# Kernel tuning notes

Hardware: AMD Instinct MI355X
Metric: run time of the kernel (lower is better)

The kernel has to match this reference:

```python
import jax, jax.numpy as jnp
import numpy as np

N_NODES = 100000
N_EDGES = 3200000
N_FEAT = 512
HIDDEN = 16
N_LABELS = 64


def gcn_layer(x, frm, to, W, b, n_nodes):
    # Original removes existing self-loops then adds one self-loop per node.
    # Equivalent jit-friendly form: zero-mask self-loop edges, add +1 to every
    # node's degree and an explicit self-loop term deg^-0.5 * deg^-0.5 * xw.
    mask = (frm != to).astype(x.dtype)                      # [E]
    deg = jax.ops.segment_sum(mask, to, num_segments=n_nodes) + 1.0  # [N], >=1 so no inf
    dis = deg ** -0.5                                        # [N]
    ew = dis[frm] * mask * dis[to]                           # [E]
    xw = x @ W                                               # [N, out]
    msgs = xw[frm] * ew[:, None]                             # gather-multiply  [E, out]
    agg = jax.ops.segment_sum(msgs, to, num_segments=n_nodes)  # scatter-add [N, out]
    out = agg + xw * (dis * dis)[:, None] + b                # self-loop weight = dis[i]^2
    return out


def setup_inputs() -> dict:
    key = jax.random.key(0)
    k1, k2, k3, k4 = jax.random.split(key, 4)
    x = jax.random.normal(k1, (N_NODES, N_FEAT), dtype=jnp.float32)
    edge_index = jax.random.randint(k2, (2, N_EDGES), 0, N_NODES, dtype=jnp.int32)
    # Xavier-uniform linear weights, zero bias (reset_paramters)
    lim1 = float(np.sqrt(6.0 / (N_FEAT + HIDDEN)))
    W1 = jax.random.uniform(k3, (N_FEAT, HIDDEN), jnp.float32, -lim1, lim1)
    b1 = jnp.zeros((HIDDEN,), jnp.float32)
    lim2 = float(np.sqrt(6.0 / (HIDDEN + N_LABELS)))
    W2 = jax.random.uniform(k4, (HIDDEN, N_LABELS), jnp.float32, -lim2, lim2)
    b2 = jnp.zeros((N_LABELS,), jnp.float32)
    return {"x": x, "edge_index": edge_index, "W1": W1, "b1": b1, "W2": W2, "b2": b2}


def reference(x, edge_index, W1, b1, W2, b2):
    n = x.shape[0]
    frm, to = edge_index[0], edge_index[1]
    h = jax.nn.relu(gcn_layer(x, frm, to, W1, b1, n))
    # dropout is identity in eval mode
    logits = gcn_layer(h, frm, to, W2, b2, n)
    return jax.nn.log_softmax(logits, axis=1)
```

## Files before the change

### kernel.cpp

```cpp
#include <hip/hip_runtime.h>
#include <hip/hip_fp16.h>
#include <cstdint>
#include <cstddef>

#define N_NODES 100000
#define N_FEAT  512
#define HIDDEN  16
#define N_LABELS 64
#define N_EDGES 3200000

#define NB    782
#define NPAD  (NB * 128)
#define CAP   4608
#define EPB   4096
#define BIN_BLOCKS 782
#define SPLITK 4
#define GBLK  196

static const size_t O_GCUR = 0;
static const size_t O_DIS  = (size_t)16 << 10;
static const size_t O_STA  = (size_t)420 << 10;
static const size_t O_END  = (size_t)824 << 10;
static const size_t O_XWS  = (size_t)1228 << 10;
static const size_t O_HS   = (size_t)4360 << 10;
static const size_t O_TMP  = (size_t)7492 << 10;
static const size_t O_PART = (size_t)21572 << 10;
#define PART_STRIDE_H ((size_t)NPAD * 16)

struct BinSh {
    unsigned short barr[EPB];
    unsigned       pk[EPB];
    int hist[NB + 1];
    int gbase[NB];
    int lcur[NB];
};
union SMemBG {
    BinSh bin;
    float xs[512 * 17];
};

__global__ __launch_bounds__(512) void k_bg(const int* __restrict__ frm,
                                            const int* __restrict__ to,
                                            int* __restrict__ gcur,
                                            unsigned* __restrict__ tmp,
                                            const float* __restrict__ x,
                                            const float* __restrict__ W1,
                                            __half* __restrict__ part) {
    __shared__ SMemBG sm;
    const int t = threadIdx.x;
    const int bid = blockIdx.x;

    if (bid < BIN_BLOCKS) {
        BinSh& B = sm.bin;
        const size_t e0 = (size_t)bid * EPB;

        for (int i = t; i < NB + 1; i += 512) B.hist[i] = 0;
        __syncthreads();

        #pragma unroll
        for (int i = t; i < EPB; i += 512) {
            size_t e = e0 + i;
            int b = NB;
            unsigned pk = 0;
            if (e < N_EDGES) {
                int f = frm[e], tt = to[e];
                if (f != tt) {
                    b = tt >> 7;
                    pk = ((unsigned)f << 7) | (unsigned)(tt & 127);
                }
            }
            B.barr[i] = (unsigned short)b;
            B.pk[i] = pk;
            atomicAdd(&B.hist[b], 1);
        }
        __syncthreads();

        for (int b = t; b < NB; b += 512) {
            B.gbase[b] = atomicAdd(&gcur[b], B.hist[b]);
            B.lcur[b] = 0;
        }
        __syncthreads();

        #pragma unroll
        for (int i = t; i < EPB; i += 512) {
            int b = B.barr[i];
            if (b < NB) {
                int r = atomicAdd(&B.lcur[b], 1);
                int p = B.gbase[b] + r;
                if (p < CAP)
                    tmp[(size_t)b * CAP + p] = B.pk[i];
            }
        }
    } else {
        const int g = bid - BIN_BLOCKS;
        const int split = g / GBLK;
        const int bx = g - split * GBLK;
        const int base = bx * 512;
        const int kb = split * 128;

        float acc[HIDDEN];
        #pragma unroll
        for (int j = 0; j < HIDDEN; ++j) acc[j] = 0.f;

        const int pr = t >> 2;
        const int pc = (t & 3) << 2;

        for (int kt = 0; kt < 8; ++kt) {
            __syncthreads();
            #pragma unroll
            for (int p = 0; p < 4; ++p) {
                int r = p * 128 + pr;
                int n = base + r;
                float4 v = make_float4(0.f, 0.f, 0.f, 0.f);
                if (n < N_NODES)
                    v = *(const float4*)(x + (size_t)n * N_FEAT + kb + kt * 16 + pc);
                sm.xs[r * 17 + pc + 0] = v.x;
                sm.xs[r * 17 + pc + 1] = v.y;
                sm.xs[r * 17 + pc + 2] = v.z;
                sm.xs[r * 17 + pc + 3] = v.w;
            }
            __syncthreads();
            #pragma unroll
            for (int kk = 0; kk < 16; ++kk) {
                float xv = sm.xs[t * 17 + kk];
                const float4* wr = (const float4*)(W1 + ((size_t)(kb + kt * 16 + kk) << 4));
                float4 wa = wr[0], wb = wr[1], wc = wr[2], wd = wr[3];
                acc[ 0] = fmaf(xv, wa.x, acc[ 0]);
                acc[ 1] = fmaf(xv, wa.y, acc[ 1]);
                acc[ 2] = fmaf(xv, wa.z, acc[ 2]);
                acc[ 3] = fmaf(xv, wa.w, acc[ 3]);
                acc[ 4] = fmaf(xv, wb.x, acc[ 4]);
                acc[ 5] = fmaf(xv, wb.y, acc[ 5]);
                acc[ 6] = fmaf(xv, wb.z, acc[ 6]);
                acc[ 7] = fmaf(xv, wb.w, acc[ 7]);
                acc[ 8] = fmaf(xv, wc.x, acc[ 8]);
                acc[ 9] = fmaf(xv, wc.y, acc[ 9]);
                acc[10] = fmaf(xv, wc.z, acc[10]);
                acc[11] = fmaf(xv, wc.w, acc[11]);
                acc[12] = fmaf(xv, wd.x, acc[12]);
                acc[13] = fmaf(xv, wd.y, acc[13]);
                acc[14] = fmaf(xv, wd.z, acc[14]);
                acc[15] = fmaf(xv, wd.w, acc[15]);
            }
        }
        int n = base + t;
        if (n < N_NODES) {
            __half2 h2[8];
            #pragma unroll
            for (int j = 0; j < 8; ++j)
                h2[j] = __float22half2_rn(make_float2(acc[2 * j], acc[2 * j + 1]));
            float4* o = (float4*)(part + (size_t)split * PART_STRIDE_H + (size_t)n * HIDDEN);
            o[0] = *(float4*)&h2[0];
            o[1] = *(float4*)&h2[4];
        }
    }
}

__global__ __launch_bounds__(512) void k_sort(unsigned* __restrict__ tmp,
                                              const int* __restrict__ gcur,
                                              int* __restrict__ starts,
                                              int* __restrict__ ends,
                                              float* __restrict__ dis) {
    __shared__ unsigned stage[CAP];
    __shared__ int cnt[128];
    __shared__ int sc[128];
    __shared__ int lcur[128];
    const int t = threadIdx.x, b = blockIdx.x;
    const int n_e = min(gcur[b], CAP);
    unsigned* seg = tmp + (size_t)b * CAP;

    if (t < 128) { cnt[t] = 0; lcur[t] = 0; }
    __syncthreads();

    for (int i = t; i < n_e; i += 512) {
        unsigned w = seg[i];
        stage[i] = w;
        atomicAdd(&cnt[w & 127u], 1);
    }
    __syncthreads();

    if (t < 128) sc[t] = cnt[t];
    __syncthreads();
    #pragma unroll
    for (int off = 1; off < 128; off <<= 1) {
        int a = 0;
        if (t < 128 && t >= off) a = sc[t - off];
        __syncthreads();
        if (t < 128) sc[t] += a;
        __syncthreads();
    }

    if (t < 128) {
        int excl = sc[t] - cnt[t];
        int node = b * 128 + t;
        int s0 = b * CAP + excl;
        starts[node] = s0;
        ends[node]   = s0 + cnt[t];
        dis[node]    = rsqrtf((float)cnt[t] + 1.0f);
    }
    __syncthreads();

    for (int i = t; i < n_e; i += 512) {
        unsigned w = stage[i];
        int tl = (int)(w & 127u);
        int p = atomicAdd(&lcur[tl], 1);
        seg[(sc[tl] - cnt[tl]) + p] = w >> 7;
    }
}

__global__ __launch_bounds__(256) void k_comb(const __half2* __restrict__ part2,
                                              const float* __restrict__ dis,
                                              __half2* __restrict__ xws2) {
    int i = blockIdx.x * 256 + threadIdx.x;
    if (i >= N_NODES * 8) return;
    const size_t st = (size_t)NPAD * 8;
    float2 a = __half22float2(part2[i]);
    float2 b = __half22float2(part2[st + i]);
    float2 c = __half22float2(part2[2 * st + i]);
    float2 d = __half22float2(part2[3 * st + i]);
    float dn = dis[i >> 3];
    xws2[i] = __float22half2_rn(make_float2(dn * (a.x + b.x + c.x + d.x),
                                            dn * (a.y + b.y + c.y + d.y)));
}

__global__ __launch_bounds__(512) void k_agg(const __half* __restrict__ rows,
                                             const unsigned* __restrict__ sorted,
                                             const int* __restrict__ starts,
                                             const int* __restrict__ ends,
                                             const float* __restrict__ dis,
                                             const float* __restrict__ bias,
                                             __half* __restrict__ outp,
                                             int mode) {
    const int t = threadIdx.x;
    const int lane = t & 15, g = t >> 4;
    const int n = blockIdx.x * 32 + g;
    const int s0 = starts[n], e0 = ends[n];
    float acc = 0.f;
    for (int base = s0; base < e0; base += 16) {
        int idx = base + lane;
        unsigned f = (idx < e0) ? sorted[idx] : 0u;
        int cnt = min(16, e0 - base);
        #pragma unroll
        for (int q = 0; q < 16; ++q) {
            unsigned fq = __shfl(f, q, 16);
            float v = __half2float(rows[(size_t)fq * HIDDEN + lane]);
            if (q < cnt) acc += v;
        }
    }
    if (n < N_NODES) {
        float dn = dis[n];
        float sum = acc + __half2float(rows[(size_t)n * HIDDEN + lane]);
        float v;
        if (mode) v = fmaxf(fmaf(dn, sum, bias[lane]), 0.f) * dn;
        else      v = dn * sum;
        outp[(size_t)n * HIDDEN + lane] = __float2half(v);
    }
}

__global__ __launch_bounds__(256) void k_out(const __half* __restrict__ z,
                                             const float* __restrict__ W2,
                                             const float* __restrict__ b2,
                                             float* __restrict__ out) {
    int gt = blockIdx.x * 256 + threadIdx.x;
    int n = gt >> 6;
    int j = gt & 63;
    float acc = b2[j];
    const __half* zr = z + (size_t)n * HIDDEN;
    #pragma unroll
    for (int k = 0; k < HIDDEN; ++k)
        acc = fmaf(__half2float(zr[k]), W2[k * N_LABELS + j], acc);
    float m = acc;
    #pragma unroll
    for (int off = 32; off > 0; off >>= 1)
        m = fmaxf(m, __shfl_xor(m, off, 64));
    float ex = __expf(acc - m);
    float sum = ex;
    #pragma unroll
    for (int off = 32; off > 0; off >>= 1)
        sum += __shfl_xor(sum, off, 64);
    out[(size_t)n * N_LABELS + j] = acc - m - __logf(sum);
}

extern "C" void kernel_launch(void* const* d_in, const int* in_sizes, int n_in,
                              void* d_out, int out_size, void* d_ws, size_t ws_size,
                              hipStream_t stream) {
    const float* x  = (const float*)d_in[0];
    const int*   ei = (const int*)d_in[1];
    const float* W1 = (const float*)d_in[2];
    const float* b1 = (const float*)d_in[3];
    const float* W2 = (const float*)d_in[4];
    const float* b2 = (const float*)d_in[5];
    float* out = (float*)d_out;
    char*  ws  = (char*)d_ws;

    int*      gcur   = (int*)(ws + O_GCUR);
    float*    dis    = (float*)(ws + O_DIS);
    int*      starts = (int*)(ws + O_STA);
    int*      ends   = (int*)(ws + O_END);
    __half*   xws    = (__half*)(ws + O_XWS);
    __half*   hs     = (__half*)(ws + O_HS);
    unsigned* tmp    = (unsigned*)(ws + O_TMP);
    __half*   part   = (__half*)(ws + O_PART);

    const int* frm = ei;
    const int* to  = ei + N_EDGES;

    hipMemsetAsync(gcur, 0, NB * sizeof(int), stream);

    k_bg   <<<BIN_BLOCKS + SPLITK * GBLK, 512, 0, stream>>>(frm, to, gcur, tmp, x, W1, part);
    k_sort <<<NB, 512, 0, stream>>>(tmp, gcur, starts, ends, dis);
    k_comb <<<3125, 256, 0, stream>>>((const __half2*)part, dis, (__half2*)xws);
    k_agg  <<<NPAD / 32, 512, 0, stream>>>(xws, tmp, starts, ends, dis, b1, hs, 1);
    k_agg  <<<NPAD / 32, 512, 0, stream>>>(hs, tmp, starts, ends, dis, b1, xws, 0);
    k_out  <<<N_NODES / 4, 256, 0, stream>>>(xws, W2, b2, out);
}
```

Measured before the change: 457.4 us.

## Replace binned sort with degree-count, block-scan offsets and global atomic scatter CSR build

Swaps the two-pass bin-then-sort CSR construction for a simpler scheme. It counts per-node in-degree with global atomics, computes per-node offsets with a block scan plus a global atomic base, then scatters source indices with per-node atomic cursors. The partial-sum combine kernel is merged into the scatter kernel as extra blocks, which saves one launch and drops the fixed CAP limit per bin. The cost is a second full read of the edge list and far more global atomics, which are contended and randomly addressed. The edge order within each node also becomes nondeterministic, and blocks receive their base offsets in arbitrary order.

Result: slower. 798.6 us (+74.6%).

```diff
diff --git a/kernel.cpp b/kernel.cpp
--- a/kernel.cpp
+++ b/kernel.cpp
@@ -11,88 +11,46 @@
 
 #define NB    782
 #define NPAD  (NB * 128)
-#define CAP   4608
 #define EPB   4096
-#define BIN_BLOCKS 782
+#define DEG_BLOCKS 782
+#define SC_BLOCKS  782
 #define SPLITK 4
 #define GBLK  196
 
-static const size_t O_GCUR = 0;
-static const size_t O_DIS  = (size_t)16 << 10;
-static const size_t O_STA  = (size_t)420 << 10;
-static const size_t O_END  = (size_t)824 << 10;
-static const size_t O_XWS  = (size_t)1228 << 10;
-static const size_t O_HS   = (size_t)4360 << 10;
-static const size_t O_TMP  = (size_t)7492 << 10;
-static const size_t O_PART = (size_t)21572 << 10;
+static const size_t O_CNT  = 0;
+static const size_t O_DEG  = (size_t)16 << 10;
+static const size_t O_DIS  = (size_t)420 << 10;
+static const size_t O_STA  = (size_t)824 << 10;
+static const size_t O_END  = (size_t)1228 << 10;
+static const size_t O_CUR  = (size_t)1632 << 10;
+static const size_t O_XWS  = (size_t)2036 << 10;
+static const size_t O_HS   = (size_t)5168 << 10;
+static const size_t O_TMP  = (size_t)8300 << 10;
+static const size_t O_PART = (size_t)20900 << 10;
 #define PART_STRIDE_H ((size_t)NPAD * 16)
-
-struct BinSh {
-    unsigned short barr[EPB];
-    unsigned       pk[EPB];
-    int hist[NB + 1];
-    int gbase[NB];
-    int lcur[NB];
-};
-union SMemBG {
-    BinSh bin;
-    float xs[512 * 17];
-};
 
 __global__ __launch_bounds__(512) void k_bg(const int* __restrict__ frm,
                                             const int* __restrict__ to,
-                                            int* __restrict__ gcur,
-                                            unsigned* __restrict__ tmp,
+                                            int* __restrict__ deg,
                                             const float* __restrict__ x,
                                             const float* __restrict__ W1,
                                             __half* __restrict__ part) {
-    __shared__ SMemBG sm;
+    __shared__ float xs[512 * 17];
     const int t = threadIdx.x;
     const int bid = blockIdx.x;
 
-    if (bid < BIN_BLOCKS) {
-        BinSh& B = sm.bin;
+    if (bid < DEG_BLOCKS) {
         const size_t e0 = (size_t)bid * EPB;
-
-        for (int i = t; i < NB + 1; i += 512) B.hist[i] = 0;
-        __syncthreads();
-
         #pragma unroll
         for (int i = t; i < EPB; i += 512) {
             size_t e = e0 + i;
-            int b = NB;
-            unsigned pk = 0;
             if (e < N_EDGES) {
                 int f = frm[e], tt = to[e];
-                if (f != tt) {
-                    b = tt >> 7;
-                    pk = ((unsigned)f << 7) | (unsigned)(tt & 127);
-                }
-            }
-            B.barr[i] = (unsigned short)b;
-            B.pk[i] = pk;
-            atomicAdd(&B.hist[b], 1);
-        }
-        __syncthreads();
-
-        for (int b = t; b < NB; b += 512) {
-            B.gbase[b] = atomicAdd(&gcur[b], B.hist[b]);
-            B.lcur[b] = 0;
-        }
-        __syncthreads();
-
-        #pragma unroll
-        for (int i = t; i < EPB; i += 512) {
-            int b = B.barr[i];
-            if (b < NB) {
-                int r = atomicAdd(&B.lcur[b], 1);
-                int p = B.gbase[b] + r;
-                if (p < CAP)
-                    tmp[(size_t)b * CAP + p] = B.pk[i];
+                if (f != tt) atomicAdd(&deg[tt], 1);
             }
         }
     } else {
-        const int g = bid - BIN_BLOCKS;
+        const int g = bid - DEG_BLOCKS;
         const int split = g / GBLK;
         const int bx = g - split * GBLK;
         const int base = bx * 512;
@@ -114,15 +72,15 @@
                 float4 v = make_float4(0.f, 0.f, 0.f, 0.f);
                 if (n < N_NODES)
                     v = *(const float4*)(x + (size_t)n * N_FEAT + kb + kt * 16 + pc);
-                sm.xs[r * 17 + pc + 0] = v.x;
-                sm.xs[r * 17 + pc + 1] = v.y;
-                sm.xs[r * 17 + pc + 2] = v.z;
-                sm.xs[r * 17 + pc + 3] = v.w;
+                xs[r * 17 + pc + 0] = v.x;
+                xs[r * 17 + pc + 1] = v.y;
+                xs[r * 17 + pc + 2] = v.z;
+                xs[r * 17 + pc + 3] = v.w;
             }
             __syncthreads();
             #pragma unroll
             for (int kk = 0; kk < 16; ++kk) {
-                float xv = sm.xs[t * 17 + kk];
+                float xv = xs[t * 17 + kk];
                 const float4* wr = (const float4*)(W1 + ((size_t)(kb + kt * 16 + kk) << 4));
                 float4 wa = wr[0], wb = wr[1], wc = wr[2], wd = wr[3];
                 acc[ 0] = fmaf(xv, wa.x, acc[ 0]);
@@ -156,75 +114,78 @@
     }
 }
 
-__global__ __launch_bounds__(512) void k_sort(unsigned* __restrict__ tmp,
-                                              const int* __restrict__ gcur,
+__global__ __launch_bounds__(128) void k_base(const int* __restrict__ deg,
+                                              int* __restrict__ cnt,
                                               int* __restrict__ starts,
                                               int* __restrict__ ends,
+                                              int* __restrict__ cur,
                                               float* __restrict__ dis) {
-    __shared__ unsigned stage[CAP];
-    __shared__ int cnt[128];
     __shared__ int sc[128];
-    __shared__ int lcur[128];
-    const int t = threadIdx.x, b = blockIdx.x;
-    const int n_e = min(gcur[b], CAP);
-    unsigned* seg = tmp + (size_t)b * CAP;
-
-    if (t < 128) { cnt[t] = 0; lcur[t] = 0; }
+    __shared__ int base;
+    const int t = threadIdx.x;
+    const int n = blockIdx.x * 128 + t;
+    const int d = deg[n];
+    sc[t] = d;
     __syncthreads();
-
-    for (int i = t; i < n_e; i += 512) {
-        unsigned w = seg[i];
-        stage[i] = w;
-        atomicAdd(&cnt[w & 127u], 1);
-    }
+    #pragma unroll
+    for (int off = 1; off < 128; off <<= 1) {
+        int a = (t >= off) ? sc[t - off] : 0;
+        __syncthreads();
+        sc[t] += a;
+        __syncthreads();
+    }
+    if (t == 127) base = atomicAdd(cnt, sc[127]);
     __syncthreads();
-
-    if (t < 128) sc[t] = cnt[t];
-    __syncthreads();
-    #pragma unroll
-    for (int off = 1; off < 128; off <<= 1) {
-        int a = 0;
-        if (t < 128 && t >= off) a = sc[t - off];
-        __syncthreads();
-        if (t < 128) sc[t] += a;
-        __syncthreads();
-    }
-
-    if (t < 128) {
-        int excl = sc[t] - cnt[t];
-        int node = b * 128 + t;
-        int s0 = b * CAP + excl;
-        starts[node] = s0;
-        ends[node]   = s0 + cnt[t];
-        dis[node]    = rsqrtf((float)cnt[t] + 1.0f);
-    }
-    __syncthreads();
-
-    for (int i = t; i < n_e; i += 512) {
-        unsigned w = stage[i];
-        int tl = (int)(w & 127u);
-        int p = atomicAdd(&lcur[tl], 1);
-        seg[(sc[tl] - cnt[tl]) + p] = w >> 7;
-    }
-}
-
-__global__ __launch_bounds__(256) void k_comb(const __half2* __restrict__ part2,
-                                              const float* __restrict__ dis,
-                                              __half2* __restrict__ xws2) {
-    int i = blockIdx.x * 256 + threadIdx.x;
-    if (i >= N_NODES * 8) return;
-    const size_t st = (size_t)NPAD * 8;
-    float2 a = __half22float2(part2[i]);
-    float2 b = __half22float2(part2[st + i]);
-    float2 c = __half22float2(part2[2 * st + i]);
-    float2 d = __half22float2(part2[3 * st + i]);
-    float dn = dis[i >> 3];
-    xws2[i] = __float22half2_rn(make_float2(dn * (a.x + b.x + c.x + d.x),
-                                            dn * (a.y + b.y + c.y + d.y)));
+    const int s0 = base + sc[t] - d;
+    starts[n] = s0;
+    ends[n]   = s0 + d;
+    cur[n]    = s0;
+    dis[n]    = rsqrtf((float)d + 1.0f);
+}
+
+__global__ __launch_bounds__(512) void k_sc(const int* __restrict__ frm,
+                                            const int* __restrict__ to,
+                                            int* __restrict__ cur,
+                                            int* __restrict__ tmp,
+                                            const __half2* __restrict__ part2,
+                                            const float* __restrict__ dis,
+                                            __half2* __restrict__ xws2) {
+    const int t = threadIdx.x;
+    const int bid = blockIdx.x;
+    if (bid < SC_BLOCKS) {
+        const size_t e0 = (size_t)bid * EPB;
+        #pragma unroll
+        for (int i = t; i < EPB; i += 512) {
+            size_t e = e0 + i;
+            if (e < N_EDGES) {
+                int f = frm[e], tt = to[e];
+                if (f != tt) {
+                    int p = atomicAdd(&cur[tt], 1);
+                    tmp[p] = f;
+                }
+            }
+        }
+    } else {
+        const int g = bid - SC_BLOCKS;
+        const size_t st = (size_t)NPAD * 8;
+        int i = g * 512 + t;
+        #pragma unroll
+        for (int rep = 0; rep < 2; ++rep, i += SC_BLOCKS * 512) {
+            if (i < N_NODES * 8) {
+                float2 a = __half22float2(part2[i]);
+                float2 b = __half22float2(part2[st + i]);
+                float2 c = __half22float2(part2[2 * st + i]);
+                float2 d = __half22float2(part2[3 * st + i]);
+                float dn = dis[i >> 3];
+                xws2[i] = __float22half2_rn(make_float2(dn * (a.x + b.x + c.x + d.x),
+                                                        dn * (a.y + b.y + c.y + d.y)));
+            }
+        }
+    }
 }
 
 __global__ __launch_bounds__(512) void k_agg(const __half* __restrict__ rows,
-                                             const unsigned* __restrict__ sorted,
+                                             const int* __restrict__ sorted,
                                              const int* __restrict__ starts,
                                              const int* __restrict__ ends,
                                              const float* __restrict__ dis,
@@ -238,7 +199,7 @@
     float acc = 0.f;
     for (int base = s0; base < e0; base += 16) {
         int idx = base + lane;
-        unsigned f = (idx < e0) ? sorted[idx] : 0u;
+        unsigned f = (idx < e0) ? (unsigned)sorted[idx] : 0u;
         int cnt = min(16, e0 - base);
         #pragma unroll
         for (int q = 0; q < 16; ++q) {
@@ -293,23 +254,26 @@
     float* out = (float*)d_out;
     char*  ws  = (char*)d_ws;
 
-    int*      gcur   = (int*)(ws + O_GCUR);
+    int*      cnt    = (int*)(ws + O_CNT);
+    int*      deg    = (int*)(ws + O_DEG);
     float*    dis    = (float*)(ws + O_DIS);
     int*      starts = (int*)(ws + O_STA);
     int*      ends   = (int*)(ws + O_END);
+    int*      cur    = (int*)(ws + O_CUR);
     __half*   xws    = (__half*)(ws + O_XWS);
     __half*   hs     = (__half*)(ws + O_HS);
-    unsigned* tmp    = (unsigned*)(ws + O_TMP);
+    int*      tmp    = (int*)(ws + O_TMP);
     __half*   part   = (__half*)(ws + O_PART);
 
     const int* frm = ei;
     const int* to  = ei + N_EDGES;
 
-    hipMemsetAsync(gcur, 0, NB * sizeof(int), stream);
-
-    k_bg   <<<BIN_BLOCKS + SPLITK * GBLK, 512, 0, stream>>>(frm, to, gcur, tmp, x, W1, part);
-    k_sort <<<NB, 512, 0, stream>>>(tmp, gcur, starts, ends, dis);
-    k_comb <<<3125, 256, 0, stream>>>((const __half2*)part, dis, (__half2*)xws);
+    hipMemsetAsync(ws, 0, O_DEG + (size_t)NPAD * sizeof(int), stream);
+
+    k_bg   <<<DEG_BLOCKS + SPLITK * GBLK, 512, 0, stream>>>(frm, to, deg, x, W1, part);
+    k_base <<<NB, 128, 0, stream>>>(deg, cnt, starts, ends, cur, dis);
+    k_sc   <<<SC_BLOCKS * 2, 512, 0, stream>>>(frm, to, cur, tmp,
+                                               (const __half2*)part, dis, (__half2*)xws);
     k_agg  <<<NPAD / 32, 512, 0, stream>>>(xws, tmp, starts, ends, dis, b1, hs, 1);
     k_agg  <<<NPAD / 32, 512, 0, stream>>>(hs, tmp, starts, ends, dis, b1, xws, 0);
     k_out  <<<N_NODES / 4, 256, 0, stream>>>(xws, W2, b2, out);
```

## Drop per-node sort; aggregate bucketed edges via shared-memory atomics

Applied to the files above, without the earlier changes.

Removes the k_sort kernel that counting-sorted each 128-node bucket into CSR order. k_agg now works one block per bucket: it walks the unsorted edges and accumulates gathered rows into a padded shared-memory tile with atomics. Node degrees are now counted with global atomics during binning, and the normalisation factor is recomputed from them where needed. This saves a kernel launch and a global read/write pass over the edges. In exchange it adds 3.2M global atomics in k_bg and shared-memory atomic contention in both aggregation passes, and k_agg launches far fewer, larger blocks (782 instead of about 3100).

After: 1.134 ms. 148% more time.

```diff
diff --git a/kernel.cpp b/kernel.cpp
--- a/kernel.cpp
+++ b/kernel.cpp
@@ -18,13 +18,11 @@
 #define GBLK  196
 
 static const size_t O_GCUR = 0;
-static const size_t O_DIS  = (size_t)16 << 10;
-static const size_t O_STA  = (size_t)420 << 10;
-static const size_t O_END  = (size_t)824 << 10;
-static const size_t O_XWS  = (size_t)1228 << 10;
-static const size_t O_HS   = (size_t)4360 << 10;
-static const size_t O_TMP  = (size_t)7492 << 10;
-static const size_t O_PART = (size_t)21572 << 10;
+static const size_t O_DEG  = (size_t)16 << 10;
+static const size_t O_XWS  = (size_t)420 << 10;
+static const size_t O_HS   = (size_t)3560 << 10;
+static const size_t O_TMP  = (size_t)6700 << 10;
+static const size_t O_PART = (size_t)20800 << 10;
 #define PART_STRIDE_H ((size_t)NPAD * 16)
 
 struct BinSh {
@@ -42,6 +40,7 @@
 __global__ __launch_bounds__(512) void k_bg(const int* __restrict__ frm,
                                             const int* __restrict__ to,
                                             int* __restrict__ gcur,
+                                            int* __restrict__ deg,
                                             unsigned* __restrict__ tmp,
                                             const float* __restrict__ x,
                                             const float* __restrict__ W1,
@@ -67,6 +66,7 @@
                 if (f != tt) {
                     b = tt >> 7;
                     pk = ((unsigned)f << 7) | (unsigned)(tt & 127);
+                    atomicAdd(&deg[tt], 1);
                 }
             }
             B.barr[i] = (unsigned short)b;
@@ -156,60 +156,8 @@
     }
 }
 
-__global__ __launch_bounds__(512) void k_sort(unsigned* __restrict__ tmp,
-                                              const int* __restrict__ gcur,
-                                              int* __restrict__ starts,
-                                              int* __restrict__ ends,
-                                              float* __restrict__ dis) {
-    __shared__ unsigned stage[CAP];
-    __shared__ int cnt[128];
-    __shared__ int sc[128];
-    __shared__ int lcur[128];
-    const int t = threadIdx.x, b = blockIdx.x;
-    const int n_e = min(gcur[b], CAP);
-    unsigned* seg = tmp + (size_t)b * CAP;
-
-    if (t < 128) { cnt[t] = 0; lcur[t] = 0; }
-    __syncthreads();
-
-    for (int i = t; i < n_e; i += 512) {
-        unsigned w = seg[i];
-        stage[i] = w;
-        atomicAdd(&cnt[w & 127u], 1);
-    }
-    __syncthreads();
-
-    if (t < 128) sc[t] = cnt[t];
-    __syncthreads();
-    #pragma unroll
-    for (int off = 1; off < 128; off <<= 1) {
-        int a = 0;
-        if (t < 128 && t >= off) a = sc[t - off];
-        __syncthreads();
-        if (t < 128) sc[t] += a;
-        __syncthreads();
-    }
-
-    if (t < 128) {
-        int excl = sc[t] - cnt[t];
-        int node = b * 128 + t;
-        int s0 = b * CAP + excl;
-        starts[node] = s0;
-        ends[node]   = s0 + cnt[t];
-        dis[node]    = rsqrtf((float)cnt[t] + 1.0f);
-    }
-    __syncthreads();
-
-    for (int i = t; i < n_e; i += 512) {
-        unsigned w = stage[i];
-        int tl = (int)(w & 127u);
-        int p = atomicAdd(&lcur[tl], 1);
-        seg[(sc[tl] - cnt[tl]) + p] = w >> 7;
-    }
-}
-
 __global__ __launch_bounds__(256) void k_comb(const __half2* __restrict__ part2,
-                                              const float* __restrict__ dis,
+                                              const int* __restrict__ deg,
                                               __half2* __restrict__ xws2) {
     int i = blockIdx.x * 256 + threadIdx.x;
     if (i >= N_NODES * 8) return;
@@ -218,42 +166,48 @@
     float2 b = __half22float2(part2[st + i]);
     float2 c = __half22float2(part2[2 * st + i]);
     float2 d = __half22float2(part2[3 * st + i]);
-    float dn = dis[i >> 3];
+    float dn = rsqrtf((float)deg[i >> 3] + 1.0f);
     xws2[i] = __float22half2_rn(make_float2(dn * (a.x + b.x + c.x + d.x),
                                             dn * (a.y + b.y + c.y + d.y)));
 }
 
 __global__ __launch_bounds__(512) void k_agg(const __half* __restrict__ rows,
-                                             const unsigned* __restrict__ sorted,
-                                             const int* __restrict__ starts,
-                                             const int* __restrict__ ends,
-                                             const float* __restrict__ dis,
+                                             const unsigned* __restrict__ tmp,
+                                             const int* __restrict__ gcur,
+                                             const int* __restrict__ deg,
                                              const float* __restrict__ bias,
                                              __half* __restrict__ outp,
                                              int mode) {
+    __shared__ float acc[128 * 17];
     const int t = threadIdx.x;
+    const int b = blockIdx.x;
+    const int n_e = min(gcur[b], CAP);
+    const unsigned* seg = tmp + (size_t)b * CAP;
+
+    #pragma unroll
+    for (int i = t; i < 128 * 17; i += 512) acc[i] = 0.f;
+    __syncthreads();
+
     const int lane = t & 15, g = t >> 4;
-    const int n = blockIdx.x * 32 + g;
-    const int s0 = starts[n], e0 = ends[n];
-    float acc = 0.f;
-    for (int base = s0; base < e0; base += 16) {
-        int idx = base + lane;
-        unsigned f = (idx < e0) ? sorted[idx] : 0u;
-        int cnt = min(16, e0 - base);
-        #pragma unroll
-        for (int q = 0; q < 16; ++q) {
-            unsigned fq = __shfl(f, q, 16);
-            float v = __half2float(rows[(size_t)fq * HIDDEN + lane]);
-            if (q < cnt) acc += v;
-        }
+    for (int i = g; i < n_e; i += 32) {
+        unsigned w = seg[i];
+        float v = __half2float(rows[(size_t)(w >> 7) * HIDDEN + lane]);
+        atomicAdd(&acc[(w & 127u) * 17 + lane], v);
     }
-    if (n < N_NODES) {
-        float dn = dis[n];
-        float sum = acc + __half2float(rows[(size_t)n * HIDDEN + lane]);
-        float v;
-        if (mode) v = fmaxf(fmaf(dn, sum, bias[lane]), 0.f) * dn;
-        else      v = dn * sum;
-        outp[(size_t)n * HIDDEN + lane] = __float2half(v);
+    __syncthreads();
+
+    #pragma unroll
+    for (int i = t; i < 2048; i += 512) {
+        int nl = i >> 4, ln = i & 15;
+        int n = b * 128 + nl;
+        if (n < N_NODES) {
+            float dn = rsqrtf((float)deg[n] + 1.0f);
+            float sum = acc[nl * 17 + ln] + __half2float(rows[(size_t)n * HIDDEN + ln]);
+            float v;
+            if (mode) v = fmaxf(fmaf(dn, sum, bias[ln]), 0.f) * dn;
+            else      v = dn * sum;
+            outp[(size_t)n * HIDDEN + ln] = __float2half(v);
+        }
     }
 }
 
@@ -293,24 +247,21 @@
     float* out = (float*)d_out;
     char*  ws  = (char*)d_ws;
 
-    int*      gcur   = (int*)(ws + O_GCUR);
-    float*    dis    = (float*)(ws + O_DIS);
-    int*      starts = (int*)(ws + O_STA);
-    int*      ends   = (int*)(ws + O_END);
-    __half*   xws    = (__half*)(ws + O_XWS);
-    __half*   hs     = (__half*)(ws + O_HS);
-    unsigned* tmp    = (unsigned*)(ws + O_TMP);
-    __half*   part   = (__half*)(ws + O_PART);
+    int*      gcur = (int*)(ws + O_GCUR);
+    int*      deg  = (int*)(ws + O_DEG);
+    __half*   xws  = (__half*)(ws + O_XWS);
+    __half*   hs   = (__half*)(ws + O_HS);
+    unsigned* tmp  = (unsigned*)(ws + O_TMP);
+    __half*   part = (__half*)(ws + O_PART);
 
     const int* frm = ei;
     const int* to  = ei + N_EDGES;
 
-    hipMemsetAsync(gcur, 0, NB * sizeof(int), stream);
-
-    k_bg   <<<BIN_BLOCKS + SPLITK * GBLK, 512, 0, stream>>>(frm, to, gcur, tmp, x, W1, part);
-    k_sort <<<NB, 512, 0, stream>>>(tmp, gcur, starts, ends, dis);
-    k_comb <<<3125, 256, 0, stream>>>((const __half2*)part, dis, (__half2*)xws);
-    k_agg  <<<NPAD / 32, 512, 0, stream>>>(xws, tmp, starts, ends, dis, b1, hs, 1);
-    k_agg  <<<NPAD / 32, 512, 0, stream>>>(hs, tmp, starts, ends, dis, b1, xws, 0);
+    hipMemsetAsync(ws, 0, O_DEG + (size_t)NPAD * sizeof(int), stream);
+
+    k_bg   <<<BIN_BLOCKS + SPLITK * GBLK, 512, 0, stream>>>(frm, to, gcur, deg, tmp, x, W1, part);
+    k_comb <<<3125, 256, 0, stream>>>((const __half2*)part, deg, (__half2*)xws);
+    k_agg  <<<NB, 512, 0, stream>>>(xws, tmp, gcur, deg, b1, hs, 1);
+    k_agg  <<<NB, 512, 0, stream>>>(hs, tmp, gcur, deg, b1, xws, 0);
     k_out  <<<N_NODES / 4, 256, 0, stream>>>(xws, W2, b2, out);
 }
```

## Fuse second aggregation with output linear and log-softmax; reuse histogram rank

Applied to the files above, without the earlier changes.

The second aggregation kernel now also does the 16x64 output projection, bias and log-softmax in registers using sub-warp shuffles. This removes the separate output kernel and the round trip of the intermediate half-precision node features through global memory. The binning phase also records each edge's rank from the histogram atomic, so the second shared-memory atomic pass and the lcur array go away. The cost is an extra rank array in shared memory, and the fused kernel does more work per thread.

Result: faster. 445.6 us (-2.6%).

```diff
diff --git a/kernel.cpp b/kernel.cpp
--- a/kernel.cpp
+++ b/kernel.cpp
@@ -29,10 +29,10 @@
 
 struct BinSh {
     unsigned short barr[EPB];
+    unsigned short rank[EPB];
     unsigned       pk[EPB];
     int hist[NB + 1];
     int gbase[NB];
-    int lcur[NB];
 };
 union SMemBG {
     BinSh bin;
@@ -69,24 +69,22 @@
                     pk = ((unsigned)f << 7) | (unsigned)(tt & 127);
                 }
             }
+            int r = atomicAdd(&B.hist[b], 1);
             B.barr[i] = (unsigned short)b;
-            B.pk[i] = pk;
-            atomicAdd(&B.hist[b], 1);
-        }
-        __syncthreads();
-
-        for (int b = t; b < NB; b += 512) {
+            B.rank[i] = (unsigned short)r;
+            B.pk[i]   = pk;
+        }
+        __syncthreads();
+
+        for (int b = t; b < NB; b += 512)
             B.gbase[b] = atomicAdd(&gcur[b], B.hist[b]);
-            B.lcur[b] = 0;
-        }
         __syncthreads();
 
         #pragma unroll
         for (int i = t; i < EPB; i += 512) {
             int b = B.barr[i];
             if (b < NB) {
-                int r = atomicAdd(&B.lcur[b], 1);
-                int p = B.gbase[b] + r;
+                int p = B.gbase[b] + (int)B.rank[i];
                 if (p < CAP)
                     tmp[(size_t)b * CAP + p] = B.pk[i];
             }
@@ -223,14 +221,13 @@
                                             dn * (a.y + b.y + c.y + d.y)));
 }
 
-__global__ __launch_bounds__(512) void k_agg(const __half* __restrict__ rows,
-                                             const unsigned* __restrict__ sorted,
-                                             const int* __restrict__ starts,
-                                             const int* __restrict__ ends,
-                                             const float* __restrict__ dis,
-                                             const float* __restrict__ bias,
-                                             __half* __restrict__ outp,
-                                             int mode) {
+__global__ __launch_bounds__(512) void k_agg1(const __half* __restrict__ rows,
+                                              const unsigned* __restrict__ sorted,
+                                              const int* __restrict__ starts,
+                                              const int* __restrict__ ends,
+                                              const float* __restrict__ dis,
+                                              const float* __restrict__ bias,
+                                              __half* __restrict__ outp) {
     const int t = threadIdx.x;
     const int lane = t & 15, g = t >> 4;
     const int n = blockIdx.x * 32 + g;
@@ -250,35 +247,65 @@
     if (n < N_NODES) {
         float dn = dis[n];
         float sum = acc + __half2float(rows[(size_t)n * HIDDEN + lane]);
-        float v;
-        if (mode) v = fmaxf(fmaf(dn, sum, bias[lane]), 0.f) * dn;
-        else      v = dn * sum;
+        float v = fmaxf(fmaf(dn, sum, bias[lane]), 0.f) * dn;
         outp[(size_t)n * HIDDEN + lane] = __float2half(v);
     }
 }
 
-__global__ __launch_bounds__(256) void k_out(const __half* __restrict__ z,
-                                             const float* __restrict__ W2,
-                                             const float* __restrict__ b2,
-                                             float* __restrict__ out) {
-    int gt = blockIdx.x * 256 + threadIdx.x;
-    int n = gt >> 6;
-    int j = gt & 63;
-    float acc = b2[j];
-    const __half* zr = z + (size_t)n * HIDDEN;
+__global__ __launch_bounds__(512) void k_agg2o(const __half* __restrict__ rows,
+                                               const unsigned* __restrict__ sorted,
+                                               const int* __restrict__ starts,
+                                               const int* __restrict__ ends,
+                                               const float* __restrict__ dis,
+                                               const float* __restrict__ W2,
+                                               const float* __restrict__ b2,
+                                               float* __restrict__ out) {
+    const int t = threadIdx.x;
+    const int lane = t & 15, g = t >> 4;
+    const int n = blockIdx.x * 32 + g;
+    const int s0 = starts[n], e0 = ends[n];
+    float acc = 0.f;
+    for (int base = s0; base < e0; base += 16) {
+        int idx = base + lane;
+        unsigned f = (idx < e0) ? sorted[idx] : 0u;
+        int cnt = min(16, e0 - base);
+        #pragma unroll
+        for (int q = 0; q < 16; ++q) {
+            unsigned fq = __shfl(f, q, 16);
+            float v = __half2float(rows[(size_t)fq * HIDDEN + lane]);
+            if (q < cnt) acc += v;
+        }
+    }
+    float dn = (n < N_NODES) ? dis[n] : 1.f;
+    float z = dn * (acc + __half2float(rows[(size_t)n * HIDDEN + lane]));
+
+    float o0 = b2[lane], o1 = b2[lane + 16], o2 = b2[lane + 32], o3 = b2[lane + 48];
     #pragma unroll
-    for (int k = 0; k < HIDDEN; ++k)
-        acc = fmaf(__half2float(zr[k]), W2[k * N_LABELS + j], acc);
-    float m = acc;
+    for (int k = 0; k < HIDDEN; ++k) {
+        float zk = __shfl(z, k, 16);
+        const float* wr = W2 + k * N_LABELS;
+        o0 = fmaf(zk, wr[lane],      o0);
+        o1 = fmaf(zk, wr[lane + 16], o1);
+        o2 = fmaf(zk, wr[lane + 32], o2);
+        o3 = fmaf(zk, wr[lane + 48], o3);
+    }
+    float m = fmaxf(fmaxf(o0, o1), fmaxf(o2, o3));
     #pragma unroll
-    for (int off = 32; off > 0; off >>= 1)
-        m = fmaxf(m, __shfl_xor(m, off, 64));
-    float ex = __expf(acc - m);
-    float sum = ex;
+    for (int off = 8; off > 0; off >>= 1)
+        m = fmaxf(m, __shfl_xor(m, off, 16));
+    float s = __expf(o0 - m) + __expf(o1 - m) + __expf(o2 - m) + __expf(o3 - m);
     #pragma unroll
-    for (int off = 32; off > 0; off >>= 1)
-        sum += __shfl_xor(sum, off, 64);
-    out[(size_t)n * N_LABELS + j] = acc - m - __logf(sum);
+    for (int off = 8; off > 0; off >>= 1)
+        s += __shfl_xor(s, off, 16);
+    float ls = m + __logf(s);
+
+    if (n < N_NODES) {
+        float* orow = out + (size_t)n * N_LABELS;
+        orow[lane]      = o0 - ls;
+        orow[lane + 16] = o1 - ls;
+        orow[lane + 32] = o2 - ls;
+        orow[lane + 48] = o3 - ls;
+    }
 }
 
 extern "C" void kernel_launch(void* const* d_in, const int* in_sizes, int n_in,
@@ -307,10 +334,9 @@
 
     hipMemsetAsync(gcur, 0, NB * sizeof(int), stream);
 
-    k_bg   <<<BIN_BLOCKS + SPLITK * GBLK, 512, 0, stream>>>(frm, to, gcur, tmp, x, W1, part);
-    k_sort <<<NB, 512, 0, stream>>>(tmp, gcur, starts, ends, dis);
-    k_comb <<<3125, 256, 0, stream>>>((const __half2*)part, dis, (__half2*)xws);
-    k_agg  <<<NPAD / 32, 512, 0, stream>>>(xws, tmp, starts, ends, dis, b1, hs, 1);
-    k_agg  <<<NPAD / 32, 512, 0, stream>>>(hs, tmp, starts, ends, dis, b1, xws, 0);
-    k_out  <<<N_NODES / 4, 256, 0, stream>>>(xws, W2, b2, out);
-}
+    k_bg    <<<BIN_BLOCKS + SPLITK * GBLK, 512, 0, stream>>>(frm, to, gcur, tmp, x, W1, part);
+    k_sort  <<<NB, 512, 0, stream>>>(tmp, gcur, starts, ends, dis);
+    k_comb  <<<3125, 256, 0, stream>>>((const __half2*)part, dis, (__half2*)xws);
+    k_agg1  <<<NPAD / 32, 512, 0, stream>>>(xws, tmp, starts, ends, dis, b1, hs);
+    k_agg2o <<<NPAD / 32, 512, 0, stream>>>(hs, tmp, starts, ends, dis, W2, b2, out);
+}
```
